# Kernel tuning notes

Hardware: AMD Instinct MI355X
Metric: run time of the kernel (lower is better)

Reference implementation:

```python
import jax, jax.numpy as jnp
import numpy as np

B, L = 1, 320
CS, CZ, CH, H, PQ, PV = 384, 128, 16, 12, 4, 8
INF, EPS = 1e5, 1e-8


def _quat_to_rot(q):
    w, x, y, z = q[..., 0], q[..., 1], q[..., 2], q[..., 3]
    r0 = jnp.stack([1 - 2*(y*y + z*z), 2*(x*y - w*z), 2*(x*z + w*y)], -1)
    r1 = jnp.stack([2*(x*y + w*z), 1 - 2*(x*x + z*z), 2*(y*z - w*x)], -1)
    r2 = jnp.stack([2*(x*z - w*y), 2*(y*z + w*x), 1 - 2*(x*x + y*y)], -1)
    return jnp.stack([r0, r1, r2], -2)


def setup_inputs():
    key = jax.random.key(0)
    ks = jax.random.split(key, 12)

    def lin(k, fan_in, fan_out):
        k1, k2 = jax.random.split(k)
        lim = 1.0 / np.sqrt(fan_in)
        return (jax.random.uniform(k1, (fan_in, fan_out), minval=-lim, maxval=lim, dtype=jnp.float32),
                jax.random.uniform(k2, (fan_out,), minval=-lim, maxval=lim, dtype=jnp.float32))

    s = jax.random.normal(ks[0], (B, L, CS), dtype=jnp.float32)
    quat = jax.random.normal(ks[1], (B, L, 4), dtype=jnp.float32)
    quat = quat / jnp.linalg.norm(quat, axis=-1, keepdims=True)
    rot = _quat_to_rot(quat)                                   # proper rotations (B,L,3,3)
    trans = 10.0 * jax.random.normal(ks[2], (B, L, 3), dtype=jnp.float32)
    z = jax.random.normal(ks[3], (B, L, L, CZ), dtype=jnp.float32)
    frame_mask = jnp.ones((B, L), dtype=jnp.float32)

    Wq, bq = lin(ks[4], CS, CH * H)
    Wkv, bkv = lin(ks[5], CS, 2 * CH * H)
    Wqp, bqp = lin(ks[6], CS, 6 * H * PQ)
    Wkvp, bkvp = lin(ks[7], CS, 6 * H * (PQ + PV))
    Wg, bg = lin(ks[8], CS, H * PQ)
    geom_weights = jnp.ones((3,), jnp.float32)
    dir_weight = jnp.asarray(0.5, jnp.float32)
    head_weights = 0.02 * jax.random.normal(ks[9], (H,), dtype=jnp.float32)
    concat_dim = H * (CH + 7 * PV) + H * CZ                    # 2400
    Wo, bo = lin(ks[10], concat_dim, CS)
    return dict(s=s, rot=rot, trans=trans, z=z, frame_mask=frame_mask,
                Wq=Wq, bq=bq, Wkv=Wkv, bkv=bkv, Wqp=Wqp, bqp=bqp,
                Wkvp=Wkvp, bkvp=bkvp, Wg=Wg, bg=bg,
                geom_weights=geom_weights, dir_weight=dir_weight,
                head_weights=head_weights, Wo=Wo, bo=bo)


def reference(s, rot, trans, z, frame_mask, Wq, bq, Wkv, bkv, Wqp, bqp,
              Wkvp, bkvp, Wg, bg, geom_weights, dir_weight, head_weights, Wo, bo):
    def proc_pts(pts_flat, P):
        # (B,L,6*H*P) -> rotate coords+translate, rotate dirs -> (B,L,H,P,6)
        pts = pts_flat.reshape(B, L, H, P, 6)
        coords = jnp.einsum('blij,blhpj->blhpi', rot, pts[..., :3]) + trans[:, :, None, None, :]
        dirs = jnp.einsum('blij,blhpj->blhpi', rot, pts[..., 3:])
        return jnp.concatenate([coords, dirs], -1)

    q = (s @ Wq + bq).reshape(B, L, H, CH)
    kv = s @ Wkv + bkv
    k = kv[..., :CH * H].reshape(B, L, H, CH)
    v = kv[..., CH * H:].reshape(B, L, H, CH)

    q_pts = proc_pts(s @ Wqp + bqp, PQ)
    kv_pts = s @ Wkvp + bkvp
    k_pts = proc_pts(kv_pts[..., :6 * H * PQ], PQ)
    v_pts = proc_pts(kv_pts[..., 6 * H * PQ:], PV)

    gate = jax.nn.sigmoid(s @ Wg + bg).reshape(B, L, H, PQ, 1)
    q_pts = q_pts * gate

    scalar_att = jnp.einsum('bqhc,bkhc->bhqk', q, k) / np.sqrt(CH).astype(np.float32)

    # position attention: per-pair point distances + log + inverse, mean over points
    delta = q_pts[:, :, None, :, :, :3] - k_pts[:, None, :, :, :, :3]   # (B,Lq,Lk,H,PQ,3)
    d = jnp.linalg.norm(delta, axis=-1)
    pos_att = (d + jnp.log(d + EPS) + 1.0 / (d + EPS)).mean(-1).transpose(0, 3, 1, 2)

    # direction attention: per-point dot minus cross-product 'curvature'
    qd, kd = q_pts[..., 3:], k_pts[..., 3:]
    dot = jnp.einsum('bqhpd,bkhpd->bqkhp', qd, kd)                       # (B,Lq,Lk,H,P)
    cr = jnp.cross(qd[:, :, None, :, None, :, :], kd[:, None, :, :, :, None, :])  # (B,Lq,Lk,H,Pk,Pq,3)
    cross = jnp.linalg.norm(cr, axis=-1).mean(-1)                        # (B,Lq,Lk,H,Pk)
    nq = jnp.linalg.norm(qd, axis=-1)[:, :, None]                        # (B,Lq,1,H,P)
    nk = jnp.linalg.norm(kd, axis=-1)[:, None]                           # (B,1,Lk,H,P)
    dir_att = (dot - cross / (nq * nk + EPS)).mean(-1).transpose(0, 3, 1, 2)

    att = scalar_att + dir_weight * (geom_weights[0] * pos_att + geom_weights[1] * dir_att)
    att = att * head_weights[:, None, None]
    mask2d = frame_mask[:, None, None, :] * frame_mask[:, None, :, None]  # (B,1,L,L)
    att = jax.nn.softmax(att + INF * (mask2d - 1.0), axis=-1)

    o_scalar = jnp.einsum('bhqk,bkhc->bqhc', att, v)
    o_geom = jnp.einsum('bhqk,bkhpd->bqhpd', att, v_pts)                 # (B,L,H,PV,6)

    # map aggregated geometry back into local frames
    rotT = jnp.swapaxes(rot, -1, -2)
    trans_inv = -jnp.einsum('blij,blj->bli', rotT, trans)
    lc = jnp.einsum('blij,blhpj->blhpi', rotT, o_geom[..., :3]) + trans_inv[:, :, None, None, :]
    ld = jnp.einsum('blij,blhpj->blhpi', rotT, o_geom[..., 3:6])
    ld = ld / jnp.maximum(jnp.linalg.norm(ld, axis=-1, keepdims=True), 1e-12)  # F.normalize
    ln = jnp.linalg.norm(lc, axis=-1, keepdims=True)
    o_geom7 = jnp.concatenate([lc, ld, ln], -1)                          # (B,L,H,PV,7)

    o_pair = jnp.einsum('bhij,bijk->bihk', att, z)                       # (B,L,H,CZ)
    out = jnp.concatenate([o_scalar.reshape(B, L, H * CH),
                           o_geom7.reshape(B, L, H * PV * 7),
                           o_pair.reshape(B, L, H * CZ)], -1)
    return out @ Wo + bo
```

## Files before the change

### kernel.cpp

```cpp
#include <hip/hip_runtime.h>
#include <hip/hip_bf16.h>
#include <math.h>

#define LSEQ 320
#define CS 384
#define CZ 128
#define CH 16
#define NH 12
#define PQ 4
#define PV 8
#define EPSF 1e-8f

typedef short short8 __attribute__((ext_vector_type(8)));
typedef float f32x4 __attribute__((ext_vector_type(4)));
typedef unsigned short ush2 __attribute__((ext_vector_type(2)));

__device__ __forceinline__ unsigned short f2b(float x) {
    union { float f; unsigned u; } v; v.f = x;
    unsigned r = (v.u + 0x7FFF + ((v.u >> 16) & 1)) >> 16;
    return (unsigned short)r;
}
__device__ __forceinline__ float b2f(unsigned short h) {
    union { unsigned u; float f; } v; v.u = ((unsigned)h) << 16;
    return v.f;
}

#define OFF_Q       0
#define OFF_KV      61440
#define OFF_QPT     184320
#define OFF_ATTHI   552960
#define OFF_ATTLO   1372160
#define OFF_CCHI    2191360
#define OFF_CCLO    2575360
#define OFF_SHI     2959360
#define OFF_SMID    2990080
#define OFF_SLO     3020800
#define OFF_WCATHI  3051520
#define OFF_WCATMID 3392512
#define OFF_WCATLO  3733504
#define OFF_BCAT    4074496
#define OFF_WOHI    4076272
#define OFF_WOLO    4537072
#define OFF_VKVHI   4997872
#define OFF_VKVLO   5120752
#define OFF_QPR     5243632
#define OFF_KVPR    5335792
#define OFF_GATE    5612272
#define OFF_PART    5627632
#define OFF_KROW    6242032
#define OFF_WCTHI   6426352
#define OFF_WCTMID  6767344
#define OFF_WCTLO   7108336
#define OFF_WOTHI   7449328
#define OFF_WOTLO   7910128

__global__ __launch_bounds__(256) void k_cast(
    const float* __restrict__ s,
    const float* __restrict__ Wq, const float* __restrict__ bq,
    const float* __restrict__ Wkv, const float* __restrict__ bkv,
    const float* __restrict__ Wqp, const float* __restrict__ bqp,
    const float* __restrict__ Wkvp, const float* __restrict__ bkvp,
    const float* __restrict__ Wg, const float* __restrict__ bg,
    const float* __restrict__ Wo,
    unsigned short* __restrict__ s_hi, unsigned short* __restrict__ s_mid,
    unsigned short* __restrict__ s_lo,
    unsigned short* __restrict__ w_hi, unsigned short* __restrict__ w_mid,
    unsigned short* __restrict__ w_lo,
    float* __restrict__ bcat,
    unsigned short* __restrict__ wo_hi, unsigned short* __restrict__ wo_lo,
    float* __restrict__ ph_hi, float* __restrict__ ph_lo)
{
    int i = blockIdx.x * 256 + threadIdx.x;
    if (i < 122880) {
        float x = s[i];
        unsigned short hi = f2b(x);
        float r1 = x - b2f(hi);
        unsigned short mid = f2b(r1);
        s_hi[i] = hi; s_mid[i] = mid; s_lo[i] = f2b(r1 - b2f(mid));
        return;
    }
    i -= 122880;
    if (i < 681984) {
        int k = i / 1776, c = i - k * 1776;
        float v;
        if (c < 192)       v = Wq[(size_t)k * 192 + c];
        else if (c < 576)  v = Wkv[(size_t)k * 384 + c - 192];
        else if (c < 864)  v = Wqp[(size_t)k * 288 + c - 576];
        else if (c < 1728) v = Wkvp[(size_t)k * 864 + c - 864];
        else               v = Wg[(size_t)k * 48 + c - 1728];
        unsigned short hi = f2b(v);
        float r1 = v - b2f(hi);
        unsigned short mid = f2b(r1);
        w_hi[i] = hi; w_mid[i] = mid; w_lo[i] = f2b(r1 - b2f(mid));
        return;
    }
    i -= 681984;
    if (i < 1776) {
        float v;
        if (i < 192)       v = bq[i];
        else if (i < 576)  v = bkv[i - 192];
        else if (i < 864)  v = bqp[i - 576];
        else if (i < 1728) v = bkvp[i - 864];
        else               v = bg[i - 1728];
        bcat[i] = v;
        return;
    }
    i -= 1776;
    if (i < 921600) {
        float v = Wo[i];
        unsigned short hi = f2b(v);
        wo_hi[i] = hi; wo_lo[i] = f2b(v - b2f(hi));
        return;
    }
    i -= 921600;
    if (i < 204800) { ph_hi[i] = 0.0f; return; }
    i -= 204800;
    if (i < 204800) ph_lo[i] = 0.0f;
}

__global__ __launch_bounds__(256) void k_tr(
    const unsigned short* __restrict__ wc_hi, const unsigned short* __restrict__ wc_mid,
    const unsigned short* __restrict__ wc_lo,
    const unsigned short* __restrict__ wo_hi, const unsigned short* __restrict__ wo_lo,
    unsigned short* __restrict__ wcT_hi, unsigned short* __restrict__ wcT_mid,
    unsigned short* __restrict__ wcT_lo,
    unsigned short* __restrict__ woT_hi, unsigned short* __restrict__ woT_lo)
{
    int m = blockIdx.z;
    const unsigned short* in; unsigned short* outp; int R, C;
    if (m == 0)      { in = wc_hi;  outp = wcT_hi;  R = 384;  C = 1776; }
    else if (m == 1) { in = wc_mid; outp = wcT_mid; R = 384;  C = 1776; }
    else if (m == 2) { in = wc_lo;  outp = wcT_lo;  R = 384;  C = 1776; }
    else if (m == 3) { in = wo_hi;  outp = woT_hi;  R = 2400; C = 384;  }
    else             { in = wo_lo;  outp = woT_lo;  R = 2400; C = 384;  }
    int r0 = blockIdx.x * 64, c0 = blockIdx.y * 64;
    if (r0 >= R || c0 >= C) return;
    __shared__ unsigned short t[64][65];
    int tid = threadIdx.x;
    #pragma unroll
    for (int rep = 0; rep < 16; rep++) {
        int idx = rep * 256 + tid;
        int i = idx >> 6, j = idx & 63;
        if (r0 + i < R && c0 + j < C) t[i][j] = in[(size_t)(r0 + i) * C + c0 + j];
    }
    __syncthreads();
    #pragma unroll
    for (int rep = 0; rep < 16; rep++) {
        int idx = rep * 256 + tid;
        int i = idx >> 6, j = idx & 63;
        if (c0 + i < C && r0 + j < R) outp[(size_t)(c0 + i) * R + r0 + j] = t[j][i];
    }
}

__global__ __launch_bounds__(256) void k_proj(
    const unsigned short* __restrict__ s_hi, const unsigned short* __restrict__ s_mid,
    const unsigned short* __restrict__ s_lo,
    const unsigned short* __restrict__ wcT_hi, const unsigned short* __restrict__ wcT_mid,
    const unsigned short* __restrict__ wcT_lo,
    const float* __restrict__ bcat,
    float* __restrict__ qo, float* __restrict__ kvo,
    float* __restrict__ qpr, float* __restrict__ kvpr, float* __restrict__ gate)
{
    __shared__ unsigned short a_h[64][56], a_m[64][56], a_l[64][56];
    __shared__ unsigned short w_h[48][56], w_m[48][56], w_l[48][56];
    int col0 = blockIdx.x * 48, l0 = blockIdx.y * 64;
    int tid = threadIdx.x;
    int lane = tid & 63, w = tid >> 6;
    int ncol = lane & 15, blk = lane >> 4, mrow = (lane >> 4) * 4;

    float* dst; int nc, cbase; bool sig = false;
    if (col0 < 192)       { nc = 192; cbase = col0;        dst = qo;   }
    else if (col0 < 576)  { nc = 384; cbase = col0 - 192;  dst = kvo;  }
    else if (col0 < 864)  { nc = 288; cbase = col0 - 576;  dst = qpr;  }
    else if (col0 < 1728) { nc = 864; cbase = col0 - 864;  dst = kvpr; }
    else                  { nc = 48;  cbase = 0;           dst = gate; sig = true; }

    f32x4 acc[3] = {};
    for (int k0 = 0; k0 < 384; k0 += 32) {
        __syncthreads();
        {
            int row = tid >> 2, seg = tid & 3;
            size_t off = (size_t)(l0 + row) * 384 + k0 + seg * 8;
            *(short8*)&a_h[row][seg * 8] = *(const short8*)(s_hi + off);
            *(short8*)&a_m[row][seg * 8] = *(const short8*)(s_mid + off);
            *(short8*)&a_l[row][seg * 8] = *(const short8*)(s_lo + off);
        }
        if (tid < 192) {
            int row = tid >> 2, seg = tid & 3;
            size_t off = (size_t)(col0 + row) * 384 + k0 + seg * 8;
            *(short8*)&w_h[row][seg * 8] = *(const short8*)(wcT_hi + off);
            *(short8*)&w_m[row][seg * 8] = *(const short8*)(wcT_mid + off);
            *(short8*)&w_l[row][seg * 8] = *(const short8*)(wcT_lo + off);
        }
        __syncthreads();
        short8 afh = *(short8*)&a_h[w * 16 + ncol][blk * 8];
        short8 afm = *(short8*)&a_m[w * 16 + ncol][blk * 8];
        short8 afl = *(short8*)&a_l[w * 16 + ncol][blk * 8];
        #pragma unroll
        for (int s3 = 0; s3 < 3; s3++) {
            short8 bfh = *(short8*)&w_h[s3 * 16 + ncol][blk * 8];
            short8 bfm = *(short8*)&w_m[s3 * 16 + ncol][blk * 8];
            short8 bfl = *(short8*)&w_l[s3 * 16 + ncol][blk * 8];
            acc[s3] = __builtin_amdgcn_mfma_f32_16x16x32_bf16(afm, bfm, acc[s3], 0, 0, 0);
            acc[s3] = __builtin_amdgcn_mfma_f32_16x16x32_bf16(afh, bfl, acc[s3], 0, 0, 0);
            acc[s3] = __builtin_amdgcn_mfma_f32_16x16x32_bf16(afl, bfh, acc[s3], 0, 0, 0);
            acc[s3] = __builtin_amdgcn_mfma_f32_16x16x32_bf16(afh, bfm, acc[s3], 0, 0, 0);
            acc[s3] = __builtin_amdgcn_mfma_f32_16x16x32_bf16(afm, bfh, acc[s3], 0, 0, 0);
            acc[s3] = __builtin_amdgcn_mfma_f32_16x16x32_bf16(afh, bfh, acc[s3], 0, 0, 0);
        }
    }
    #pragma unroll
    for (int s3 = 0; s3 < 3; s3++) {
        float bv = bcat[col0 + s3 * 16 + ncol];
        int cloc = cbase + s3 * 16 + ncol;
        #pragma unroll
        for (int r = 0; r < 4; r++) {
            float v2 = acc[s3][r] + bv;
            if (sig) v2 = 1.0f / (1.0f + expf(-v2));
            dst[(size_t)(l0 + w * 16 + mrow + r) * nc + cloc] = v2;
        }
    }
}

__global__ __launch_bounds__(256) void k_points(
    const float* __restrict__ qpr, const float* __restrict__ kvpr, const float* __restrict__ gate,
    const float* __restrict__ rot, const float* __restrict__ trans,
    const float* __restrict__ kv,
    float* __restrict__ qpt, float* __restrict__ krow,
    unsigned short* __restrict__ vkv_hi, unsigned short* __restrict__ vkv_lo)
{
    __shared__ float vsh[96][6];
    __shared__ float kp_s[48][6];
    __shared__ float kn_s[48];
    int l = blockIdx.x, t = threadIdx.x;
    const float* R = rot + l * 9;
    float tx = trans[l * 3], ty = trans[l * 3 + 1], tz = trans[l * 3 + 2];
    if (t < 192) {
        const float* src; float g = 1.0f; float* dst = nullptr; int vj = -1, kj = -1;
        if (t < 48)      { src = qpr + (size_t)l * 288 + t * 6; g = gate[l * 48 + t]; dst = qpt + ((size_t)l * 48 + t) * 6; }
        else if (t < 96) { kj = t - 48; src = kvpr + (size_t)l * 864 + kj * 6; }
        else             { int j = t - 96; src = kvpr + (size_t)l * 864 + 288 + j * 6; vj = j; }
        float px = src[0], py = src[1], pz = src[2], ux = src[3], uy = src[4], uz = src[5];
        float c0 = R[0] * px + R[1] * py + R[2] * pz + tx;
        float c1 = R[3] * px + R[4] * py + R[5] * pz + ty;
        float c2 = R[6] * px + R[7] * py + R[8] * pz + tz;
        float d0 = R[0] * ux + R[1] * uy + R[2] * uz;
        float d1 = R[3] * ux + R[4] * uy + R[5] * uz;
        float d2 = R[6] * ux + R[7] * uy + R[8] * uz;
        if (vj >= 0) {
            vsh[vj][0] = c0; vsh[vj][1] = c1; vsh[vj][2] = c2;
            vsh[vj][3] = d0; vsh[vj][4] = d1; vsh[vj][5] = d2;
        } else if (kj >= 0) {
            kp_s[kj][0] = c0; kp_s[kj][1] = c1; kp_s[kj][2] = c2;
            kp_s[kj][3] = d0; kp_s[kj][4] = d1; kp_s[kj][5] = d2;
            kn_s[kj] = sqrtf(d0 * d0 + d1 * d1 + d2 * d2);
        } else {
            dst[0] = c0 * g; dst[1] = c1 * g; dst[2] = c2 * g;
            dst[3] = d0 * g; dst[4] = d1 * g; dst[5] = d2 * g;
        }
    }
    __syncthreads();
    #pragma unroll
    for (int e = 0; e < 3; e++) {
        int u = t * 3 + e;
        int h = u >> 6, n = u & 63;
        float val;
        if (n < 16) val = kv[(size_t)l * 384 + 192 + h * 16 + n];
        else        val = vsh[h * 8 + (n - 16) / 6][(n - 16) % 6];
        unsigned short hi = f2b(val);
        size_t idx = ((size_t)h * 64 + n) * 320 + l;
        vkv_hi[idx] = hi;
        vkv_lo[idx] = f2b(val - b2f(hi));
    }
    for (int idx = t; idx < 576; idx += 256) {
        int h = idx / 48, j = idx - h * 48;
        float v;
        if (j < 24)      v = kp_s[h * 4 + j / 6][j % 6];
        else if (j < 40) v = kv[(size_t)l * 384 + h * 16 + (j - 24)];
        else if (j < 44) v = kn_s[h * 4 + (j - 40)];
        else             v = 0.0f;
        krow[((size_t)h * 320 + l) * 48 + j] = v;
    }
}

__global__ __launch_bounds__(256) void k_att(
    const float* __restrict__ qb, const float* __restrict__ qpt,
    const float* __restrict__ krow,
    const float* __restrict__ fm, const float* __restrict__ gw,
    const float* __restrict__ dwp, const float* __restrict__ hwp,
    unsigned short* __restrict__ att_hi, unsigned short* __restrict__ att_lo)
{
    int tid = threadIdx.x;
    int w = tid >> 6, lane = tid & 63;
    int iq = blockIdx.x * 4 + w;
    int h = blockIdx.y;

    float qv[CH];
    #pragma unroll
    for (int c = 0; c < CH; c++) qv[c] = qb[(size_t)iq * 192 + h * CH + c];
    float qp[24];
    #pragma unroll
    for (int j = 0; j < 24; j++) qp[j] = qpt[(size_t)iq * 288 + h * 24 + j];
    float nq[PQ], nq2[PQ];
    #pragma unroll
    for (int p = 0; p < PQ; p++) {
        float x = qp[p * 6 + 3], y = qp[p * 6 + 4], zz = qp[p * 6 + 5];
        nq2[p] = x * x + y * y + zz * zz;
        nq[p] = sqrtf(nq2[p]);
    }
    float dwv = dwp[0], g0 = gw[0], g1 = gw[1], hwv = hwp[h];
    float fmi = fm[iq];

    float lg[5];
    #pragma unroll
    for (int r = 0; r < 5; r++) {
        int kk = r * 64 + lane;
        const float* row = krow + ((size_t)h * 320 + kk) * 48;

        float scalar = 0.f;
        #pragma unroll
        for (int c = 0; c < CH; c++) scalar += qv[c] * row[24 + c];
        scalar *= 0.25f;

        float pos = 0.f;
        #pragma unroll
        for (int p = 0; p < PQ; p++) {
            float dx = qp[p * 6] - row[p * 6];
            float dy = qp[p * 6 + 1] - row[p * 6 + 1];
            float dz = qp[p * 6 + 2] - row[p * 6 + 2];
            float d = __builtin_amdgcn_sqrtf(dx * dx + dy * dy + dz * dz);
            float de = d + EPSF;
            pos += d + __logf(de) + __builtin_amdgcn_rcpf(de);
        }
        pos *= 0.25f;

        float dir = 0.f;
        #pragma unroll
        for (int p = 0; p < PQ; p++) {
            float kx = row[p * 6 + 3], ky = row[p * 6 + 4], kz = row[p * 6 + 5];
            float nk = row[40 + p];
            float nk2 = nk * nk;
            float cm = 0.f, dself = 0.f;
            #pragma unroll
            for (int pq = 0; pq < PQ; pq++) {
                float dq = qp[pq * 6 + 3] * kx + qp[pq * 6 + 4] * ky + qp[pq * 6 + 5] * kz;
                if (pq == p) dself = dq;
                cm += __builtin_amdgcn_sqrtf(fmaxf(nq2[pq] * nk2 - dq * dq, 0.0f));
            }
            cm *= 0.25f;
            dir += dself - cm * __builtin_amdgcn_rcpf(nq[p] * nk + EPSF);
        }
        dir *= 0.25f;

        float logit = scalar + dwv * (g0 * pos + g1 * dir);
        logit *= hwv;
        logit += 100000.0f * (fmi * fm[kk] - 1.0f);
        lg[r] = logit;
    }

    float mx = lg[0];
    #pragma unroll
    for (int r = 1; r < 5; r++) mx = fmaxf(mx, lg[r]);
    for (int m = 32; m; m >>= 1) mx = fmaxf(mx, __shfl_xor(mx, m, 64));

    float e[5], sm = 0.f;
    #pragma unroll
    for (int r = 0; r < 5; r++) { e[r] = __expf(lg[r] - mx); sm += e[r]; }
    for (int m = 32; m; m >>= 1) sm += __shfl_xor(sm, m, 64);
    float inv = 1.0f / sm;
    #pragma unroll
    for (int r = 0; r < 5; r++) {
        float p = e[r] * inv;
        unsigned short hi = f2b(p);
        size_t idx = ((size_t)h * 320 + iq) * 320 + r * 64 + lane;
        att_hi[idx] = hi;
        att_lo[idx] = f2b(p - b2f(hi));
    }
}

__global__ __launch_bounds__(256) void k_svpair(
    const unsigned short* __restrict__ att_hi, const unsigned short* __restrict__ att_lo,
    const unsigned short* __restrict__ vkv_hi, const unsigned short* __restrict__ vkv_lo,
    const float* __restrict__ z,
    const float* __restrict__ rot, const float* __restrict__ trans,
    unsigned short* __restrict__ cc_hi, unsigned short* __restrict__ cc_lo)
{
    __shared__ unsigned short a_hi[16][56];
    __shared__ unsigned short a_lo[16][56];
    __shared__ unsigned short B[128][56];
    __shared__ float ogsh[16][49];
    int bid = blockIdx.x;
    int tid = threadIdx.x;
    int lane = tid & 63, w = tid >> 6;
    int ncol = lane & 15, blk = lane >> 4, mrow = (lane >> 4) * 4;

    if (bid < 240) {
        int iq0 = (bid % 20) * 16, h = bid / 20;
        f32x4 acc = {};
        for (int k0 = 0; k0 < 320; k0 += 32) {
            __syncthreads();
            if (tid < 64) {
                int row = tid >> 2, seg = tid & 3;
                size_t off = ((size_t)h * 320 + iq0 + row) * 320 + k0 + seg * 8;
                *(short8*)&a_hi[row][seg * 8] = *(const short8*)(att_hi + off);
                *(short8*)&a_lo[row][seg * 8] = *(const short8*)(att_lo + off);
            }
            {
                int row = tid >> 2, seg = tid & 3;
                size_t off = ((size_t)h * 64 + row) * 320 + k0 + seg * 8;
                *(short8*)&B[row][seg * 8]      = *(const short8*)(vkv_hi + off);
                *(short8*)&B[64 + row][seg * 8] = *(const short8*)(vkv_lo + off);
            }
            __syncthreads();
            short8 afh = *(short8*)&a_hi[ncol][blk * 8];
            short8 afl = *(short8*)&a_lo[ncol][blk * 8];
            short8 bfh = *(short8*)&B[w * 16 + ncol][blk * 8];
            short8 bfl = *(short8*)&B[64 + w * 16 + ncol][blk * 8];
            acc = __builtin_amdgcn_mfma_f32_16x16x32_bf16(afh, bfh, acc, 0, 0, 0);
            acc = __builtin_amdgcn_mfma_f32_16x16x32_bf16(afh, bfl, acc, 0, 0, 0);
            acc = __builtin_amdgcn_mfma_f32_16x16x32_bf16(afl, bfh, acc, 0, 0, 0);
        }
        {
            int n = w * 16 + ncol;
            #pragma unroll
            for (int r = 0; r < 4; r++) {
                int iq = iq0 + mrow + r;
                float v = acc[r];
                if (n < 16) {
                    unsigned short hi = f2b(v);
                    size_t idx = (size_t)iq * 2400 + h * 16 + n;
                    cc_hi[idx] = hi;
                    cc_lo[idx] = f2b(v - b2f(hi));
                } else {
                    ogsh[mrow + r][n - 16] = v;
                }
            }
        }
        __syncthreads();
        if (tid < 128) {
            int iqr = tid >> 3, p = tid & 7;
            int l = iq0 + iqr;
            const float* R = rot + l * 9;
            float tx = trans[l * 3], ty = trans[l * 3 + 1], tz = trans[l * 3 + 2];
            const float* o = &ogsh[iqr][p * 6];
            float gx = o[0] - tx, gy = o[1] - ty, gz = o[2] - tz;
            float l0 = R[0] * gx + R[3] * gy + R[6] * gz;
            float l1 = R[1] * gx + R[4] * gy + R[7] * gz;
            float l2 = R[2] * gx + R[5] * gy + R[8] * gz;
            float dx = o[3], dy = o[4], dz = o[5];
            float e0 = R[0] * dx + R[3] * dy + R[6] * dz;
            float e1 = R[1] * dx + R[4] * dy + R[7] * dz;
            float e2 = R[2] * dx + R[5] * dy + R[8] * dz;
            float n = sqrtf(e0 * e0 + e1 * e1 + e2 * e2);
            float inv = 1.0f / fmaxf(n, 1e-12f);
            float ln = sqrtf(l0 * l0 + l1 * l1 + l2 * l2);
            float vals[7] = { l0, l1, l2, e0 * inv, e1 * inv, e2 * inv, ln };
            size_t base = (size_t)l * 2400 + 192 + (h * PV + p) * 7;
            #pragma unroll
            for (int j = 0; j < 7; j++) {
                unsigned short hi = f2b(vals[j]);
                cc_hi[base + j] = hi;
                cc_lo[base + j] = f2b(vals[j] - b2f(hi));
            }
        }
    } else {
        int iq = bid - 240;
        f32x4 acc[2] = {};
        for (int k0 = 0; k0 < 320; k0 += 32) {
            __syncthreads();
            if (tid < 64) {
                int row = tid >> 2, seg = tid & 3;
                size_t off = (size_t)row * 102400 + (size_t)iq * 320 + k0 + seg * 8;
                *(short8*)&a_hi[row][seg * 8] = *(const short8*)(att_hi + off);
                *(short8*)&a_lo[row][seg * 8] = *(const short8*)(att_lo + off);
            }
            {
                int kp2 = (tid >> 4) * 2;
                int cb = (tid & 15) * 8;
                const float* src0 = z + ((size_t)iq * 320 + k0 + kp2) * 128 + cb;
                float4 a0 = *(const float4*)(src0);
                float4 a1 = *(const float4*)(src0 + 4);
                float4 b0 = *(const float4*)(src0 + 128);
                float4 b1 = *(const float4*)(src0 + 132);
                float va[8] = {a0.x, a0.y, a0.z, a0.w, a1.x, a1.y, a1.z, a1.w};
                float vb[8] = {b0.x, b0.y, b0.z, b0.w, b1.x, b1.y, b1.z, b1.w};
                #pragma unroll
                for (int c = 0; c < 8; c++) {
                    ush2 pr;
                    pr[0] = f2b(va[c]);
                    pr[1] = f2b(vb[c]);
                    *(ush2*)&B[cb + c][kp2] = pr;
                }
            }
            __syncthreads();
            short8 afh = *(short8*)&a_hi[ncol][blk * 8];
            short8 afl = *(short8*)&a_lo[ncol][blk * 8];
            #pragma unroll
            for (int s2 = 0; s2 < 2; s2++) {
                short8 bf = *(short8*)&B[w * 32 + s2 * 16 + ncol][blk * 8];
                acc[s2] = __builtin_amdgcn_mfma_f32_16x16x32_bf16(afl, bf, acc[s2], 0, 0, 0);
                acc[s2] = __builtin_amdgcn_mfma_f32_16x16x32_bf16(afh, bf, acc[s2], 0, 0, 0);
            }
        }
        #pragma unroll
        for (int s2 = 0; s2 < 2; s2++) {
            int n = w * 32 + s2 * 16 + ncol;
            #pragma unroll
            for (int r = 0; r < 4; r++) {
                int h = mrow + r;
                if (h < 12) {
                    float v = acc[s2][r];
                    unsigned short hi = f2b(v);
                    size_t idx = (size_t)iq * 2400 + 864 + h * 128 + n;
                    cc_hi[idx] = hi;
                    cc_lo[idx] = f2b(v - b2f(hi));
                }
            }
        }
    }
}

__global__ __launch_bounds__(256) void k_gemm(
    const unsigned short* __restrict__ cc_hi, const unsigned short* __restrict__ cc_lo,
    const unsigned short* __restrict__ woT_hi, const unsigned short* __restrict__ woT_lo,
    float* __restrict__ part)
{
    __shared__ unsigned short a_hi[64][56];
    __shared__ unsigned short a_lo[64][56];
    __shared__ unsigned short w_hi[48][56];
    __shared__ unsigned short w_lo[48][56];
    int iq0 = blockIdx.x * 64, col0 = blockIdx.y * 48, ks = blockIdx.z;
    int tid = threadIdx.x;
    int lane = tid & 63, w = tid >> 6;
    int ncol = lane & 15, blk = lane >> 4, mrow = (lane >> 4) * 4;

    f32x4 acc[3] = {};
    for (int kc = 0; kc < 15; kc++) {
        int k0 = ks * 480 + kc * 32;
        __syncthreads();
        {
            int row = tid >> 2, seg = tid & 3;
            size_t off = (size_t)(iq0 + row) * 2400 + k0 + seg * 8;
            *(short8*)&a_hi[row][seg * 8] = *(const short8*)(cc_hi + off);
            *(short8*)&a_lo[row][seg * 8] = *(const short8*)(cc_lo + off);
        }
        if (tid < 192) {
            int row = tid >> 2, seg = tid & 3;
            size_t off = (size_t)(col0 + row) * 2400 + k0 + seg * 8;
            *(short8*)&w_hi[row][seg * 8] = *(const short8*)(woT_hi + off);
            *(short8*)&w_lo[row][seg * 8] = *(const short8*)(woT_lo + off);
        }
        __syncthreads();
        short8 afh = *(short8*)&a_hi[w * 16 + ncol][blk * 8];
        short8 afl = *(short8*)&a_lo[w * 16 + ncol][blk * 8];
        #pragma unroll
        for (int s3 = 0; s3 < 3; s3++) {
            short8 bfh = *(short8*)&w_hi[s3 * 16 + ncol][blk * 8];
            short8 bfl = *(short8*)&w_lo[s3 * 16 + ncol][blk * 8];
            acc[s3] = __builtin_amdgcn_mfma_f32_16x16x32_bf16(afh, bfh, acc[s3], 0, 0, 0);
            acc[s3] = __builtin_amdgcn_mfma_f32_16x16x32_bf16(afh, bfl, acc[s3], 0, 0, 0);
            acc[s3] = __builtin_amdgcn_mfma_f32_16x16x32_bf16(afl, bfh, acc[s3], 0, 0, 0);
        }
    }
    #pragma unroll
    for (int s3 = 0; s3 < 3; s3++) {
        int cn = col0 + s3 * 16 + ncol;
        #pragma unroll
        for (int r = 0; r < 4; r++)
            part[((size_t)ks * 320 + iq0 + w * 16 + mrow + r) * 384 + cn] = acc[s3][r];
    }
}

__global__ __launch_bounds__(256) void k_reduce(
    const float* __restrict__ part, const float* __restrict__ bo, float* __restrict__ out)
{
    int i = blockIdx.x * 256 + threadIdx.x;
    float v = bo[i % CS];
    #pragma unroll
    for (int ks = 0; ks < 5; ks++) v += part[(size_t)ks * 122880 + i];
    out[i] = v;
}

extern "C" void kernel_launch(void* const* d_in, const int* in_sizes, int n_in,
                              void* d_out, int out_size, void* d_ws, size_t ws_size,
                              hipStream_t stream)
{
    const float* s     = (const float*)d_in[0];
    const float* rot   = (const float*)d_in[1];
    const float* trans = (const float*)d_in[2];
    const float* z     = (const float*)d_in[3];
    const float* fm    = (const float*)d_in[4];
    const float* Wq    = (const float*)d_in[5];
    const float* bq    = (const float*)d_in[6];
    const float* Wkv   = (const float*)d_in[7];
    const float* bkv   = (const float*)d_in[8];
    const float* Wqp   = (const float*)d_in[9];
    const float* bqp   = (const float*)d_in[10];
    const float* Wkvp  = (const float*)d_in[11];
    const float* bkvp  = (const float*)d_in[12];
    const float* Wg    = (const float*)d_in[13];
    const float* bg    = (const float*)d_in[14];
    const float* gw    = (const float*)d_in[15];
    const float* dw    = (const float*)d_in[16];
    const float* hw    = (const float*)d_in[17];
    const float* Wo    = (const float*)d_in[18];
    const float* bo    = (const float*)d_in[19];

    float* ws = (float*)d_ws;
    float*          q       = ws + OFF_Q;
    float*          kv      = ws + OFF_KV;
    float*          qpt     = ws + OFF_QPT;
    unsigned short* att_hi  = (unsigned short*)(ws + OFF_ATTHI);
    unsigned short* att_lo  = (unsigned short*)(ws + OFF_ATTLO);
    float*          ph_hi   = ws + OFF_ATTHI + 12 * 51200;
    float*          ph_lo   = ws + OFF_ATTLO + 12 * 51200;
    unsigned short* cc_hi   = (unsigned short*)(ws + OFF_CCHI);
    unsigned short* cc_lo   = (unsigned short*)(ws + OFF_CCLO);
    unsigned short* s_hi    = (unsigned short*)(ws + OFF_SHI);
    unsigned short* s_mid   = (unsigned short*)(ws + OFF_SMID);
    unsigned short* s_lo    = (unsigned short*)(ws + OFF_SLO);
    unsigned short* wc_hi   = (unsigned short*)(ws + OFF_WCATHI);
    unsigned short* wc_mid  = (unsigned short*)(ws + OFF_WCATMID);
    unsigned short* wc_lo   = (unsigned short*)(ws + OFF_WCATLO);
    float*          bcat    = ws + OFF_BCAT;
    unsigned short* wo_hi   = (unsigned short*)(ws + OFF_WOHI);
    unsigned short* wo_lo   = (unsigned short*)(ws + OFF_WOLO);
    unsigned short* vkv_hi  = (unsigned short*)(ws + OFF_VKVHI);
    unsigned short* vkv_lo  = (unsigned short*)(ws + OFF_VKVLO);
    float*          qpr     = ws + OFF_QPR;
    float*          kvpr    = ws + OFF_KVPR;
    float*          gate    = ws + OFF_GATE;
    float*          part    = ws + OFF_PART;
    float*          krow    = ws + OFF_KROW;
    unsigned short* wcT_hi  = (unsigned short*)(ws + OFF_WCTHI);
    unsigned short* wcT_mid = (unsigned short*)(ws + OFF_WCTMID);
    unsigned short* wcT_lo  = (unsigned short*)(ws + OFF_WCTLO);
    unsigned short* woT_hi  = (unsigned short*)(ws + OFF_WOTHI);
    unsigned short* woT_lo  = (unsigned short*)(ws + OFF_WOTLO);
    float* out = (float*)d_out;

    k_cast<<<dim3(8352), dim3(256), 0, stream>>>(s, Wq, bq, Wkv, bkv, Wqp, bqp,
                                                 Wkvp, bkvp, Wg, bg, Wo,
                                                 s_hi, s_mid, s_lo, wc_hi, wc_mid, wc_lo,
                                                 bcat, wo_hi, wo_lo, ph_hi, ph_lo);
    k_tr<<<dim3(38, 28, 5), dim3(256), 0, stream>>>(wc_hi, wc_mid, wc_lo, wo_hi, wo_lo,
                                                    wcT_hi, wcT_mid, wcT_lo, woT_hi, woT_lo);
    k_proj<<<dim3(37, 5), dim3(256), 0, stream>>>(s_hi, s_mid, s_lo, wcT_hi, wcT_mid, wcT_lo,
                                                  bcat, q, kv, qpr, kvpr, gate);
    k_points<<<dim3(LSEQ), dim3(256), 0, stream>>>(qpr, kvpr, gate, rot, trans, kv,
                                                   qpt, krow, vkv_hi, vkv_lo);
    k_att<<<dim3(80, NH), dim3(256), 0, stream>>>(q, qpt, krow, fm, gw, dw, hw,
                                                  att_hi, att_lo);
    k_svpair<<<dim3(560), dim3(256), 0, stream>>>(att_hi, att_lo, vkv_hi, vkv_lo, z,
                                                  rot, trans, cc_hi, cc_lo);
    k_gemm<<<dim3(5, 8, 5), dim3(256), 0, stream>>>(cc_hi, cc_lo, woT_hi, woT_lo, part);
    k_reduce<<<dim3(480), dim3(256), 0, stream>>>(part, bo, out);
}
```

Before: 216.7 us.

## Retile projection and output GEMMs, pair queries per wave in attention, remap z loads

```diff
diff --git a/kernel.cpp b/kernel.cpp
--- a/kernel.cpp
+++ b/kernel.cpp
@@ -152,7 +152,7 @@
     }
 }
 
-__global__ __launch_bounds__(256) void k_proj(
+__global__ __launch_bounds__(192) void k_proj(
     const unsigned short* __restrict__ s_hi, const unsigned short* __restrict__ s_mid,
     const unsigned short* __restrict__ s_lo,
     const unsigned short* __restrict__ wcT_hi, const unsigned short* __restrict__ wcT_mid,
@@ -161,9 +161,9 @@
     float* __restrict__ qo, float* __restrict__ kvo,
     float* __restrict__ qpr, float* __restrict__ kvpr, float* __restrict__ gate)
 {
-    __shared__ unsigned short a_h[64][56], a_m[64][56], a_l[64][56];
+    __shared__ unsigned short a_h[16][56], a_m[16][56], a_l[16][56];
     __shared__ unsigned short w_h[48][56], w_m[48][56], w_l[48][56];
-    int col0 = blockIdx.x * 48, l0 = blockIdx.y * 64;
+    int col0 = blockIdx.x * 48, l0 = blockIdx.y * 16;
     int tid = threadIdx.x;
     int lane = tid & 63, w = tid >> 6;
     int ncol = lane & 15, blk = lane >> 4, mrow = (lane >> 4) * 4;
@@ -175,17 +175,18 @@
     else if (col0 < 1728) { nc = 864; cbase = col0 - 864;  dst = kvpr; }
     else                  { nc = 48;  cbase = 0;           dst = gate; sig = true; }
 
-    f32x4 acc[3] = {};
+    f32x4 acc = {};
     for (int k0 = 0; k0 < 384; k0 += 32) {
         __syncthreads();
         {
-            int row = tid >> 2, seg = tid & 3;
+            int arr = tid >> 6, idx = tid & 63;
+            int row = idx >> 2, seg = idx & 3;
             size_t off = (size_t)(l0 + row) * 384 + k0 + seg * 8;
-            *(short8*)&a_h[row][seg * 8] = *(const short8*)(s_hi + off);
-            *(short8*)&a_m[row][seg * 8] = *(const short8*)(s_mid + off);
-            *(short8*)&a_l[row][seg * 8] = *(const short8*)(s_lo + off);
-        }
-        if (tid < 192) {
+            if (arr == 0)      *(short8*)&a_h[row][seg * 8] = *(const short8*)(s_hi + off);
+            else if (arr == 1) *(short8*)&a_m[row][seg * 8] = *(const short8*)(s_mid + off);
+            else               *(short8*)&a_l[row][seg * 8] = *(const short8*)(s_lo + off);
+        }
+        {
             int row = tid >> 2, seg = tid & 3;
             size_t off = (size_t)(col0 + row) * 384 + k0 + seg * 8;
             *(short8*)&w_h[row][seg * 8] = *(const short8*)(wcT_hi + off);
@@ -193,31 +194,28 @@
             *(short8*)&w_l[row][seg * 8] = *(const short8*)(wcT_lo + off);
         }
         __syncthreads();
-        short8 afh = *(short8*)&a_h[w * 16 + ncol][blk * 8];
-        short8 afm = *(short8*)&a_m[w * 16 + ncol][blk * 8];
-        short8 afl = *(short8*)&a_l[w * 16 + ncol][blk * 8];
-        #pragma unroll
-        for (int s3 = 0; s3 < 3; s3++) {
-            short8 bfh = *(short8*)&w_h[s3 * 16 + ncol][blk * 8];
-            short8 bfm = *(short8*)&w_m[s3 * 16 + ncol][blk * 8];
-            short8 bfl = *(short8*)&w_l[s3 * 16 + ncol][blk * 8];
-            acc[s3] = __builtin_amdgcn_mfma_f32_16x16x32_bf16(afm, bfm, acc[s3], 0, 0, 0);
-            acc[s3] = __builtin_amdgcn_mfma_f32_16x16x32_bf16(afh, bfl, acc[s3], 0, 0, 0);
-            acc[s3] = __builtin_amdgcn_mfma_f32_16x16x32_bf16(afl, bfh, acc[s3], 0, 0, 0);
-            acc[s3] = __builtin_amdgcn_mfma_f32_16x16x32_bf16(afh, bfm, acc[s3], 0, 0, 0);
-            acc[s3] = __builtin_amdgcn_mfma_f32_16x16x32_bf16(afm, bfh, acc[s3], 0, 0, 0);
-            acc[s3] = __builtin_amdgcn_mfma_f32_16x16x32_bf16(afh, bfh, acc[s3], 0, 0, 0);
-        }
-    }
-    #pragma unroll
-    for (int s3 = 0; s3 < 3; s3++) {
-        float bv = bcat[col0 + s3 * 16 + ncol];
-        int cloc = cbase + s3 * 16 + ncol;
+        short8 afh = *(short8*)&a_h[ncol][blk * 8];
+        short8 afm = *(short8*)&a_m[ncol][blk * 8];
+        short8 afl = *(short8*)&a_l[ncol][blk * 8];
+        short8 bfh = *(short8*)&w_h[w * 16 + ncol][blk * 8];
+        short8 bfm = *(short8*)&w_m[w * 16 + ncol][blk * 8];
+        short8 bfl = *(short8*)&w_l[w * 16 + ncol][blk * 8];
+        acc = __builtin_amdgcn_mfma_f32_16x16x32_bf16(afm, bfm, acc, 0, 0, 0);
+        acc = __builtin_amdgcn_mfma_f32_16x16x32_bf16(afh, bfl, acc, 0, 0, 0);
+        acc = __builtin_amdgcn_mfma_f32_16x16x32_bf16(afl, bfh, acc, 0, 0, 0);
+        acc = __builtin_amdgcn_mfma_f32_16x16x32_bf16(afh, bfm, acc, 0, 0, 0);
+        acc = __builtin_amdgcn_mfma_f32_16x16x32_bf16(afm, bfh, acc, 0, 0, 0);
+        acc = __builtin_amdgcn_mfma_f32_16x16x32_bf16(afh, bfh, acc, 0, 0, 0);
+    }
+    {
+        int n = w * 16 + ncol;
+        float bv = bcat[col0 + n];
+        int cloc = cbase + n;
         #pragma unroll
         for (int r = 0; r < 4; r++) {
-            float v2 = acc[s3][r] + bv;
+            float v2 = acc[r] + bv;
             if (sig) v2 = 1.0f / (1.0f + expf(-v2));
-            dst[(size_t)(l0 + w * 16 + mrow + r) * nc + cloc] = v2;
+            dst[(size_t)(l0 + mrow + r) * nc + cloc] = v2;
         }
     }
 }
@@ -292,87 +290,123 @@
 {
     int tid = threadIdx.x;
     int w = tid >> 6, lane = tid & 63;
-    int iq = blockIdx.x * 4 + w;
+    int iqA = blockIdx.x * 8 + w * 2;
+    int iqB = iqA + 1;
     int h = blockIdx.y;
 
-    float qv[CH];
-    #pragma unroll
-    for (int c = 0; c < CH; c++) qv[c] = qb[(size_t)iq * 192 + h * CH + c];
-    float qp[24];
-    #pragma unroll
-    for (int j = 0; j < 24; j++) qp[j] = qpt[(size_t)iq * 288 + h * 24 + j];
-    float nq[PQ], nq2[PQ];
+    float qvA[CH], qvB[CH];
+    #pragma unroll
+    for (int c = 0; c < CH; c++) {
+        qvA[c] = qb[(size_t)iqA * 192 + h * CH + c];
+        qvB[c] = qb[(size_t)iqB * 192 + h * CH + c];
+    }
+    float qpA[24], qpB[24];
+    #pragma unroll
+    for (int j = 0; j < 24; j++) {
+        qpA[j] = qpt[(size_t)iqA * 288 + h * 24 + j];
+        qpB[j] = qpt[(size_t)iqB * 288 + h * 24 + j];
+    }
+    float nqA[PQ], nq2A[PQ], nqB[PQ], nq2B[PQ];
     #pragma unroll
     for (int p = 0; p < PQ; p++) {
-        float x = qp[p * 6 + 3], y = qp[p * 6 + 4], zz = qp[p * 6 + 5];
-        nq2[p] = x * x + y * y + zz * zz;
-        nq[p] = sqrtf(nq2[p]);
+        float x = qpA[p * 6 + 3], y = qpA[p * 6 + 4], zz = qpA[p * 6 + 5];
+        nq2A[p] = x * x + y * y + zz * zz; nqA[p] = sqrtf(nq2A[p]);
+        x = qpB[p * 6 + 3]; y = qpB[p * 6 + 4]; zz = qpB[p * 6 + 5];
+        nq2B[p] = x * x + y * y + zz * zz; nqB[p] = sqrtf(nq2B[p]);
     }
     float dwv = dwp[0], g0 = gw[0], g1 = gw[1], hwv = hwp[h];
-    float fmi = fm[iq];
-
-    float lg[5];
-    #pragma unroll
+    float fmA = fm[iqA], fmB = fm[iqB];
+
+    float lgA[5], lgB[5];
     for (int r = 0; r < 5; r++) {
         int kk = r * 64 + lane;
-        const float* row = krow + ((size_t)h * 320 + kk) * 48;
-
-        float scalar = 0.f;
+        const float* rowp = krow + ((size_t)h * 320 + kk) * 48;
+        float rw[44];
         #pragma unroll
-        for (int c = 0; c < CH; c++) scalar += qv[c] * row[24 + c];
-        scalar *= 0.25f;
-
-        float pos = 0.f;
+        for (int j = 0; j < 44; j++) rw[j] = rowp[j];
+        float fmk = fm[kk];
+
         #pragma unroll
-        for (int p = 0; p < PQ; p++) {
-            float dx = qp[p * 6] - row[p * 6];
-            float dy = qp[p * 6 + 1] - row[p * 6 + 1];
-            float dz = qp[p * 6 + 2] - row[p * 6 + 2];
-            float d = __builtin_amdgcn_sqrtf(dx * dx + dy * dy + dz * dz);
-            float de = d + EPSF;
-            pos += d + __logf(de) + __builtin_amdgcn_rcpf(de);
-        }
-        pos *= 0.25f;
-
-        float dir = 0.f;
-        #pragma unroll
-        for (int p = 0; p < PQ; p++) {
-            float kx = row[p * 6 + 3], ky = row[p * 6 + 4], kz = row[p * 6 + 5];
-            float nk = row[40 + p];
-            float nk2 = nk * nk;
-            float cm = 0.f, dself = 0.f;
+        for (int which = 0; which < 2; which++) {
+            const float* qp = which ? qpB : qpA;
+            const float* qv = which ? qvB : qvA;
+            const float* nq = which ? nqB : nqA;
+            const float* nq2 = which ? nq2B : nq2A;
+            float fmi = which ? fmB : fmA;
+
+            float scalar = 0.f;
             #pragma unroll
-            for (int pq = 0; pq < PQ; pq++) {
-                float dq = qp[pq * 6 + 3] * kx + qp[pq * 6 + 4] * ky + qp[pq * 6 + 5] * kz;
-                if (pq == p) dself = dq;
-                cm += __builtin_amdgcn_sqrtf(fmaxf(nq2[pq] * nk2 - dq * dq, 0.0f));
-            }
-            cm *= 0.25f;
-            dir += dself - cm * __builtin_amdgcn_rcpf(nq[p] * nk + EPSF);
-        }
-        dir *= 0.25f;
-
-        float logit = scalar + dwv * (g0 * pos + g1 * dir);
-        logit *= hwv;
-        logit += 100000.0f * (fmi * fm[kk] - 1.0f);
-        lg[r] = logit;
-    }
-
-    float mx = lg[0];
-    #pragma unroll
-    for (int r = 1; r < 5; r++) mx = fmaxf(mx, lg[r]);
-    for (int m = 32; m; m >>= 1) mx = fmaxf(mx, __shfl_xor(mx, m, 64));
-
-    float e[5], sm = 0.f;
-    #pragma unroll
-    for (int r = 0; r < 5; r++) { e[r] = __expf(lg[r] - mx); sm += e[r]; }
-    for (int m = 32; m; m >>= 1) sm += __shfl_xor(sm, m, 64);
-    float inv = 1.0f / sm;
+            for (int c = 0; c < CH; c++) scalar += qv[c] * rw[24 + c];
+            scalar *= 0.25f;
+
+            float pos = 0.f;
+            #pragma unroll
+            for (int p = 0; p < PQ; p++) {
+                float dx = qp[p * 6] - rw[p * 6];
+                float dy = qp[p * 6 + 1] - rw[p * 6 + 1];
+                float dz = qp[p * 6 + 2] - rw[p * 6 + 2];
+                float d = __builtin_amdgcn_sqrtf(dx * dx + dy * dy + dz * dz);
+                float de = d + EPSF;
+                pos += d + __logf(de) + __builtin_amdgcn_rcpf(de);
+            }
+            pos *= 0.25f;
+
+            float dir = 0.f;
+            #pragma unroll
+            for (int p = 0; p < PQ; p++) {
+                float kx = rw[p * 6 + 3], ky = rw[p * 6 + 4], kz = rw[p * 6 + 5];
+                float nk = rw[40 + p];
+                float nk2 = nk * nk;
+                float cm = 0.f, dself = 0.f;
+                #pragma unroll
+                for (int pq = 0; pq < PQ; pq++) {
+                    float dq = qp[pq * 6 + 3] * kx + qp[pq * 6 + 4] * ky + qp[pq * 6 + 5] * kz;
+                    if (pq == p) dself = dq;
+                    cm += __builtin_amdgcn_sqrtf(fmaxf(nq2[pq] * nk2 - dq * dq, 0.0f));
+                }
+                cm *= 0.25f;
+                dir += dself - cm * __builtin_amdgcn_rcpf(nq[p] * nk + EPSF);
+            }
+            dir *= 0.25f;
+
+            float logit = scalar + dwv * (g0 * pos + g1 * dir);
+            logit *= hwv;
+            logit += 100000.0f * (fmi * fmk - 1.0f);
+            if (which) lgB[r] = logit; else lgA[r] = logit;
+        }
+    }
+
+    float mxA = lgA[0];
+    #pragma unroll
+    for (int r = 1; r < 5; r++) mxA = fmaxf(mxA, lgA[r]);
+    for (int m = 32; m; m >>= 1) mxA = fmaxf(mxA, __shfl_xor(mxA, m, 64));
+    float eA[5], smA = 0.f;
+    #pragma unroll
+    for (int r = 0; r < 5; r++) { eA[r] = __expf(lgA[r] - mxA); smA += eA[r]; }
+    for (int m = 32; m; m >>= 1) smA += __shfl_xor(smA, m, 64);
+    float invA = 1.0f / smA;
     #pragma unroll
     for (int r = 0; r < 5; r++) {
-        float p = e[r] * inv;
+        float p = eA[r] * invA;
         unsigned short hi = f2b(p);
-        size_t idx = ((size_t)h * 320 + iq) * 320 + r * 64 + lane;
+        size_t idx = ((size_t)h * 320 + iqA) * 320 + r * 64 + lane;
+        att_hi[idx] = hi;
+        att_lo[idx] = f2b(p - b2f(hi));
+    }
+    float mxB = lgB[0];
+    #pragma unroll
+    for (int r = 1; r < 5; r++) mxB = fmaxf(mxB, lgB[r]);
+    for (int m = 32; m; m >>= 1) mxB = fmaxf(mxB, __shfl_xor(mxB, m, 64));
+    float eB[5], smB = 0.f;
+    #pragma unroll
+    for (int r = 0; r < 5; r++) { eB[r] = __expf(lgB[r] - mxB); smB += eB[r]; }
+    for (int m = 32; m; m >>= 1) smB += __shfl_xor(smB, m, 64);
+    float invB = 1.0f / smB;
+    #pragma unroll
+    for (int r = 0; r < 5; r++) {
+        float p = eB[r] * invB;
+        unsigned short hi = f2b(p);
+        size_t idx = ((size_t)h * 320 + iqB) * 320 + r * 64 + lane;
         att_hi[idx] = hi;
         att_lo[idx] = f2b(p - b2f(hi));
     }
@@ -475,8 +509,8 @@
                 *(short8*)&a_lo[row][seg * 8] = *(const short8*)(att_lo + off);
             }
             {
-                int kp2 = (tid >> 4) * 2;
-                int cb = (tid & 15) * 8;
+                int kp2 = (tid & 15) * 2;
+                int cb = (tid >> 4) * 8;
                 const float* src0 = z + ((size_t)iq * 320 + k0 + kp2) * 128 + cb;
                 float4 a0 = *(const float4*)(src0);
                 float4 a1 = *(const float4*)(src0 + 4);
@@ -525,49 +559,47 @@
     const unsigned short* __restrict__ woT_hi, const unsigned short* __restrict__ woT_lo,
     float* __restrict__ part)
 {
-    __shared__ unsigned short a_hi[64][56];
-    __shared__ unsigned short a_lo[64][56];
-    __shared__ unsigned short w_hi[48][56];
-    __shared__ unsigned short w_lo[48][56];
-    int iq0 = blockIdx.x * 64, col0 = blockIdx.y * 48, ks = blockIdx.z;
+    __shared__ unsigned short a_h[16][56], a_l[16][56];
+    __shared__ unsigned short w_h[64][56], w_l[64][56];
+    int iq0 = blockIdx.x * 16, col0 = blockIdx.y * 64, ks = blockIdx.z;
     int tid = threadIdx.x;
     int lane = tid & 63, w = tid >> 6;
     int ncol = lane & 15, blk = lane >> 4, mrow = (lane >> 4) * 4;
 
-    f32x4 acc[3] = {};
+    f32x4 acc = {};
     for (int kc = 0; kc < 15; kc++) {
         int k0 = ks * 480 + kc * 32;
         __syncthreads();
-        {
-            int row = tid >> 2, seg = tid & 3;
+        if (tid < 128) {
+            int arr = tid >> 6, idx = tid & 63;
+            int row = idx >> 2, seg = idx & 3;
             size_t off = (size_t)(iq0 + row) * 2400 + k0 + seg * 8;
-            *(short8*)&a_hi[row][seg * 8] = *(const short8*)(cc_hi + off);
-            *(short8*)&a_lo[row][seg * 8] = *(const short8*)(cc_lo + off);
-        }
-        if (tid < 192) {
-            int row = tid >> 2, seg = tid & 3;
+            if (arr == 0) *(short8*)&a_h[row][seg * 8] = *(const short8*)(cc_hi + off);
+            else          *(short8*)&a_l[row][seg * 8] = *(const short8*)(cc_lo + off);
+        }
+        #pragma unroll
+        for (int t2 = 0; t2 < 2; t2++) {
+            int idx = tid * 2 + t2;
+            int arr = idx >> 8, i2 = idx & 255;
+            int row = i2 >> 2, seg = i2 & 3;
             size_t off = (size_t)(col0 + row) * 2400 + k0 + seg * 8;
-            *(short8*)&w_hi[row][seg * 8] = *(const short8*)(woT_hi + off);
-            *(short8*)&w_lo[row][seg * 8] = *(const short8*)(woT_lo + off);
+            if (arr == 0) *(short8*)&w_h[row][seg * 8] = *(const short8*)(woT_hi + off);
+            else          *(short8*)&w_l[row][seg * 8] = *(const short8*)(woT_lo + off);
         }
         __syncthreads();
-        short8 afh = *(short8*)&a_hi[w * 16 + ncol][blk * 8];
-        short8 afl = *(short8*)&a_lo[w * 16 + ncol][blk * 8];
-        #pragma unroll
-        for (int s3 = 0; s3 < 3; s3++) {
-            short8 bfh = *(short8*)&w_hi[s3 * 16 + ncol][blk * 8];
-            short8 bfl = *(short8*)&w_lo[s3 * 16 + ncol][blk * 8];
-            acc[s3] = __builtin_amdgcn_mfma_f32_16x16x32_bf16(afh, bfh, acc[s3], 0, 0, 0);
-            acc[s3] = __builtin_amdgcn_mfma_f32_16x16x32_bf16(afh, bfl, acc[s3], 0, 0, 0);
-            acc[s3] = __builtin_amdgcn_mfma_f32_16x16x32_bf16(afl, bfh, acc[s3], 0, 0, 0);
-        }
-    }
-    #pragma unroll
-    for (int s3 = 0; s3 < 3; s3++) {
-        int cn = col0 + s3 * 16 + ncol;
+        short8 afh = *(short8*)&a_h[ncol][blk * 8];
+        short8 afl = *(short8*)&a_l[ncol][blk * 8];
+        short8 bfh = *(short8*)&w_h[w * 16 + ncol][blk * 8];
+        short8 bfl = *(short8*)&w_l[w * 16 + ncol][blk * 8];
+        acc = __builtin_amdgcn_mfma_f32_16x16x32_bf16(afh, bfh, acc, 0, 0, 0);
+        acc = __builtin_amdgcn_mfma_f32_16x16x32_bf16(afh, bfl, acc, 0, 0, 0);
+        acc = __builtin_amdgcn_mfma_f32_16x16x32_bf16(afl, bfh, acc, 0, 0, 0);
+    }
+    {
+        int cn = col0 + w * 16 + ncol;
         #pragma unroll
         for (int r = 0; r < 4; r++)
-            part[((size_t)ks * 320 + iq0 + w * 16 + mrow + r) * 384 + cn] = acc[s3][r];
+            part[((size_t)ks * 320 + iq0 + mrow + r) * 384 + cn] = acc[r];
     }
 }
 
@@ -645,14 +677,14 @@
                                                  bcat, wo_hi, wo_lo, ph_hi, ph_lo);
     k_tr<<<dim3(38, 28, 5), dim3(256), 0, stream>>>(wc_hi, wc_mid, wc_lo, wo_hi, wo_lo,
                                                     wcT_hi, wcT_mid, wcT_lo, woT_hi, woT_lo);
-    k_proj<<<dim3(37, 5), dim3(256), 0, stream>>>(s_hi, s_mid, s_lo, wcT_hi, wcT_mid, wcT_lo,
-                                                  bcat, q, kv, qpr, kvpr, gate);
+    k_proj<<<dim3(37, 20), dim3(192), 0, stream>>>(s_hi, s_mid, s_lo, wcT_hi, wcT_mid, wcT_lo,
+                                                   bcat, q, kv, qpr, kvpr, gate);
     k_points<<<dim3(LSEQ), dim3(256), 0, stream>>>(qpr, kvpr, gate, rot, trans, kv,
                                                    qpt, krow, vkv_hi, vkv_lo);
-    k_att<<<dim3(80, NH), dim3(256), 0, stream>>>(q, qpt, krow, fm, gw, dw, hw,
+    k_att<<<dim3(40, NH), dim3(256), 0, stream>>>(q, qpt, krow, fm, gw, dw, hw,
                                                   att_hi, att_lo);
     k_svpair<<<dim3(560), dim3(256), 0, stream>>>(att_hi, att_lo, vkv_hi, vkv_lo, z,
                                                   rot, trans, cc_hi, cc_lo);
-    k_gemm<<<dim3(5, 8, 5), dim3(256), 0, stream>>>(cc_hi, cc_lo, woT_hi, woT_lo, part);
+    k_gemm<<<dim3(20, 6, 5), dim3(256), 0, stream>>>(cc_hi, cc_lo, woT_hi, woT_lo, part);
     k_reduce<<<dim3(480), dim3(256), 0, stream>>>(part, bo, out);
 }
```

Measured after the change: 210.0 us. 1.03x faster.
